# Kernel tuning notes

Hardware: AMD Instinct MI355X
Metric: run time of the kernel (lower is better)

The kernel has to match this reference:

```python
import jax, jax.numpy as jnp
import numpy as np

B, H, A, D = 4096, 50, 32, 64          # batch, history len, neighbor count, embed_dim
NU, NV = 100000, 100000                # num users, num items
L = H + A                              # total gathered entries per node


def setup_inputs() -> dict:
    key = jax.random.key(0)
    ks = jax.random.split(key, 16)
    # embedding tables (u2e/v2e uniform(-1,1) as in module init, r2e ~ N(0,1) default)
    u2e = jax.random.uniform(ks[0], (NU, D), minval=-1.0, maxval=1.0, dtype=jnp.float32)
    v2e = jax.random.uniform(ks[1], (NV, D), minval=-1.0, maxval=1.0, dtype=jnp.float32)
    r2e = jax.random.normal(ks[2], (7, D), dtype=jnp.float32)
    relation_att = jax.random.normal(ks[3], (2 * D,), dtype=jnp.float32)
    s = 1.0 / np.sqrt(2 * D)  # torch Linear default init bound
    agg_W = jax.random.uniform(ks[4], (D, 2 * D), minval=-s, maxval=s, dtype=jnp.float32)
    agg_b = jax.random.uniform(ks[5], (D,), minval=-s, maxval=s, dtype=jnp.float32)
    lin1_W = jax.random.uniform(ks[6], (D, 2 * D), minval=-s, maxval=s, dtype=jnp.float32)
    lin1_b = jax.random.uniform(ks[7], (D,), minval=-s, maxval=s, dtype=jnp.float32)
    nodes_u = jax.random.randint(ks[8], (B,), 0, NU)
    nodes_v = jax.random.randint(ks[9], (B,), 0, NV)
    hist_u = jax.random.randint(ks[10], (B, H), 0, NV)   # user history = items
    hist_ur = jax.random.randint(ks[11], (B, H), 0, 6)   # ratings 0..5
    adj_u = jax.random.randint(ks[12], (B, A), 0, NU)    # social neighbors = users
    hist_v = jax.random.randint(ks[13], (B, H), 0, NU)   # item history = users
    hist_vr = jax.random.randint(ks[14], (B, H), 0, 6)
    adj_v = jax.random.randint(ks[15], (B, A), 0, NV)    # item-adj neighbors = items
    return dict(u2e=u2e, v2e=v2e, r2e=r2e, relation_att=relation_att,
                agg_W=agg_W, agg_b=agg_b, lin1_W=lin1_W, lin1_b=lin1_b,
                nodes_u=nodes_u, nodes_v=nodes_v,
                hist_u=hist_u, hist_ur=hist_ur, adj_u=adj_u,
                hist_v=hist_v, hist_vr=hist_vr, adj_v=adj_v)


def _encode(node_tab, target_tab, hist_tab, neigh_tab, r2e, relation_att,
            agg_W, agg_b, lin1_W, lin1_b, nodes, targets, hn, hr, adj):
    # Node_Encoder.forward + Node_Aggregator (percent=1.0 -> deterministic:
    # multinomial selects all indices; softmax-weighted sum is permutation-invariant).
    nf = node_tab[nodes]                                   # [B, D]
    tf = target_tab[targets]                               # [B, D]
    # query (computed as in original; with percent=1 the norm-softmax sampling
    # probability does not affect the output)
    _q = jnp.concatenate([nf, tf], axis=-1) @ agg_W.T + agg_b  # [B, D]
    hist_feat = jnp.concatenate([hist_tab[hn], neigh_tab[adj]], axis=1)  # [B, L, D]
    rates = jnp.concatenate([hr, jnp.full(adj.shape, 6, dtype=hr.dtype)], axis=1)
    rate_feat = r2e[rates]                                 # [B, L, D]
    sel = jnp.concatenate([hist_feat, rate_feat], axis=-1)  # [B, L, 2D]
    logits = jnp.einsum('ble,e->bl', sel, relation_att)    # [B, L]
    p = jax.nn.softmax(logits, axis=1)                     # softmax2 over entries
    neigh = jnp.einsum('bl,bld->bd', p, hist_feat)         # weighted sum [B, D]
    comb = jnp.concatenate([nf, neigh], axis=-1)           # [B, 2D]
    return jax.nn.relu(comb @ lin1_W.T + lin1_b)           # [B, D]


def reference(u2e, v2e, r2e, relation_att, agg_W, agg_b, lin1_W, lin1_b,
              nodes_u, nodes_v, hist_u, hist_ur, adj_u, hist_v, hist_vr, adj_v):
    # user side: isitem=False -> node=u2e, target=v2e, hist=v2e, neighbor=u2e
    eu = _encode(u2e, v2e, v2e, u2e, r2e, relation_att, agg_W, agg_b, lin1_W, lin1_b,
                 nodes_u, nodes_v, hist_u, hist_ur, adj_u)
    # item side: isitem=True -> node=v2e, target=u2e, hist=u2e, neighbor=v2e
    ev = _encode(v2e, u2e, u2e, v2e, r2e, relation_att, agg_W, agg_b, lin1_W, lin1_b,
                 nodes_v, nodes_u, hist_v, hist_vr, adj_v)
    return jnp.sum(eu * ev, axis=1)                        # [B]
```

## Files before the change

### kernel.cpp

```cpp
#include <hip/hip_runtime.h>


typedef _Float16 half4v __attribute__((ext_vector_type(4)));

#define NB 4096
#define NH 50
#define NA 32
#define ND 64
#define NROWS 100000


__global__ __launch_bounds__(256) void convert_f16(const float* __restrict__ src,
                                                   _Float16* __restrict__ dst,
                                                   int n4)
{
    int i = blockIdx.x * blockDim.x + threadIdx.x;
    const int stride = gridDim.x * blockDim.x;
    const float4* s4 = (const float4*)src;
    half4v* d4 = (half4v*)dst;
    for (; i < n4; i += stride) {
        const float4 v = s4[i];
        half4v h;
        h.x = (_Float16)v.x; h.y = (_Float16)v.y;
        h.z = (_Float16)v.z; h.w = (_Float16)v.w;
        d4[i] = h;
    }
}

__global__ void rlog_setup(const float* __restrict__ r2e,
                           const float* __restrict__ ra,
                           float* __restrict__ ws_rlog)
{
    const int lane = threadIdx.x;
    const float ra_hi = ra[64 + lane];
    #pragma unroll
    for (int r = 0; r < 7; ++r) {
        float part = r2e[r * 64 + lane] * ra_hi;
        #pragma unroll
        for (int off = 32; off >= 1; off >>= 1)
            part += __shfl_xor(part, off);
        if (lane == 0) ws_rlog[r] = part;
    }
}


__global__ __launch_bounds__(256, 8) void graphconsis_f16(
    const float* __restrict__ u2e, const float* __restrict__ v2e,
    const _Float16* __restrict__ uh, const _Float16* __restrict__ vh,
    const float* __restrict__ ra,
    const float* __restrict__ lin1_W, const float* __restrict__ lin1_b,
    const int* __restrict__ nodes_u, const int* __restrict__ nodes_v,
    const int* __restrict__ hist_u, const int* __restrict__ hist_ur,
    const int* __restrict__ adj_u,
    const int* __restrict__ hist_v, const int* __restrict__ hist_vr,
    const int* __restrict__ adj_v,
    const float* __restrict__ ws_rlog,
    float* __restrict__ out)
{
    __shared__ float lds_comb[4][128];
    __shared__ float ed[4][64];

    const int wid  = threadIdx.x >> 6;
    const int lane = threadIdx.x & 63;
    const int g    = lane >> 4;
    const int j    = lane & 15;
    const int side = wid >> 1;
    const int b    = __builtin_amdgcn_readfirstlane(blockIdx.x * 2 + (wid & 1));

    const float* nodeTab      = side ? v2e : u2e;
    const _Float16* histTab   = side ? uh : vh;
    const _Float16* neighTab  = side ? vh : uh;
    const int* nodes = side ? nodes_v : nodes_u;
    const int* hn    = side ? hist_v  : hist_u;
    const int* hr    = side ? hist_vr : hist_ur;
    const int* adj   = side ? adj_v   : adj_u;

    const float4 ra4  = *(const float4*)(ra + 4 * j);
    const float rlog6 = ws_rlog[6];

    int hidx[13];
    #pragma unroll
    for (int k = 0; k < 13; ++k) {
        int l = 4 * k + g; if (l > NH - 1) l = NH - 1;
        hidx[k] = hn[b * NH + l];
    }
    float rl0 = 0.f;
    { int l = 4 * j + g; if (l < NH) rl0 = ws_rlog[hr[b * NH + l]]; }

    float ssum = 0.f;
    float4 acc = make_float4(0.f, 0.f, 0.f, 0.f);

    #pragma unroll 4
    for (int k = 0; k < 12; ++k) {
        const half4v eh = *(const half4v*)(histTab + hidx[k] * ND + 4 * j);
        const float4 e = make_float4((float)eh.x, (float)eh.y, (float)eh.z, (float)eh.w);
        float part = e.x * ra4.x;
        part = fmaf(e.y, ra4.y, part);
        part = fmaf(e.z, ra4.z, part);
        part = fmaf(e.w, ra4.w, part);
        part += (j == k) ? rl0 : 0.f;
        part += __shfl_xor(part, 1);
        part += __shfl_xor(part, 2);
        part += __shfl_xor(part, 4);
        part += __shfl_xor(part, 8);
        const float p = __expf(part);
        ssum += p;
        acc.x = fmaf(p, e.x, acc.x);
        acc.y = fmaf(p, e.y, acc.y);
        acc.z = fmaf(p, e.z, acc.z);
        acc.w = fmaf(p, e.w, acc.w);
    }
    {
        const half4v eh = *(const half4v*)(histTab + hidx[12] * ND + 4 * j);
        const float4 e = make_float4((float)eh.x, (float)eh.y, (float)eh.z, (float)eh.w);
        float part = e.x * ra4.x;
        part = fmaf(e.y, ra4.y, part);
        part = fmaf(e.z, ra4.z, part);
        part = fmaf(e.w, ra4.w, part);
        part += (j == 12) ? rl0 : 0.f;
        part += __shfl_xor(part, 1);
        part += __shfl_xor(part, 2);
        part += __shfl_xor(part, 4);
        part += __shfl_xor(part, 8);
        const float p = (g < 2) ? __expf(part) : 0.f;
        ssum += p;
        acc.x = fmaf(p, e.x, acc.x);
        acc.y = fmaf(p, e.y, acc.y);
        acc.z = fmaf(p, e.z, acc.z);
        acc.w = fmaf(p, e.w, acc.w);
    }
    #pragma unroll 4
    for (int k = 0; k < 8; ++k) {
        const int idx = adj[b * NA + 4 * k + g];
        const half4v eh = *(const half4v*)(neighTab + idx * ND + 4 * j);
        const float4 e = make_float4((float)eh.x, (float)eh.y, (float)eh.z, (float)eh.w);
        float part = e.x * ra4.x;
        part = fmaf(e.y, ra4.y, part);
        part = fmaf(e.z, ra4.z, part);
        part = fmaf(e.w, ra4.w, part);
        part += __shfl_xor(part, 1);
        part += __shfl_xor(part, 2);
        part += __shfl_xor(part, 4);
        part += __shfl_xor(part, 8);
        const float p = __expf(part + rlog6);
        ssum += p;
        acc.x = fmaf(p, e.x, acc.x);
        acc.y = fmaf(p, e.y, acc.y);
        acc.z = fmaf(p, e.z, acc.z);
        acc.w = fmaf(p, e.w, acc.w);
    }

    ssum += __shfl_xor(ssum, 16);
    ssum += __shfl_xor(ssum, 32);
    acc.x += __shfl_xor(acc.x, 16); acc.x += __shfl_xor(acc.x, 32);
    acc.y += __shfl_xor(acc.y, 16); acc.y += __shfl_xor(acc.y, 32);
    acc.z += __shfl_xor(acc.z, 16); acc.z += __shfl_xor(acc.z, 32);
    acc.w += __shfl_xor(acc.w, 16); acc.w += __shfl_xor(acc.w, 32);

    const float inv = 1.0f / ssum;
    const float4 nf4 = *(const float4*)(nodeTab + nodes[b] * ND + 4 * j);

    if (g == 0) {
        *(float4*)&lds_comb[wid][4 * j] = nf4;
        float4 n4 = make_float4(acc.x * inv, acc.y * inv, acc.z * inv, acc.w * inv);
        *(float4*)&lds_comb[wid][64 + 4 * j] = n4;
    }

    float o = lin1_b[lane];
    const float4* W4 = (const float4*)(lin1_W + lane * 128);
    const float4* C4 = (const float4*)lds_comb[wid];
    #pragma unroll 8
    for (int kk = 0; kk < 32; ++kk) {
        const float4 w = W4[kk];
        const float4 c = C4[kk];
        o = fmaf(w.x, c.x, o);
        o = fmaf(w.y, c.y, o);
        o = fmaf(w.z, c.z, o);
        o = fmaf(w.w, c.w, o);
    }
    const float evec = fmaxf(o, 0.f);

    ed[wid][lane] = evec;
    __syncthreads();

    if (wid < 2) {
        float prod = ed[wid][lane] * ed[wid + 2][lane];
        #pragma unroll
        for (int off = 32; off >= 1; off >>= 1)
            prod += __shfl_xor(prod, off);
        if (lane == 0) out[blockIdx.x * 2 + wid] = prod;
    }
}


__global__ __launch_bounds__(256, 8) void graphconsis_f32(
    const float* __restrict__ u2e, const float* __restrict__ v2e,
    const float* __restrict__ ra,
    const float* __restrict__ lin1_W, const float* __restrict__ lin1_b,
    const int* __restrict__ nodes_u, const int* __restrict__ nodes_v,
    const int* __restrict__ hist_u, const int* __restrict__ hist_ur,
    const int* __restrict__ adj_u,
    const int* __restrict__ hist_v, const int* __restrict__ hist_vr,
    const int* __restrict__ adj_v,
    const float* __restrict__ ws_rlog,
    float* __restrict__ out)
{
    __shared__ float lds_comb[4][128];
    __shared__ float ed[4][64];

    const int wid  = threadIdx.x >> 6;
    const int lane = threadIdx.x & 63;
    const int g    = lane >> 4;
    const int j    = lane & 15;
    const int side = wid >> 1;
    const int b    = __builtin_amdgcn_readfirstlane(blockIdx.x * 2 + (wid & 1));

    const float* nodeTab  = side ? v2e : u2e;
    const float* histTab  = side ? u2e : v2e;
    const float* neighTab = side ? v2e : u2e;
    const int* nodes = side ? nodes_v : nodes_u;
    const int* hn    = side ? hist_v  : hist_u;
    const int* hr    = side ? hist_vr : hist_ur;
    const int* adj   = side ? adj_v   : adj_u;

    const float4 ra4  = *(const float4*)(ra + 4 * j);
    const float rlog6 = ws_rlog[6];

    int hidx[13];
    #pragma unroll
    for (int k = 0; k < 13; ++k) {
        int l = 4 * k + g; if (l > NH - 1) l = NH - 1;
        hidx[k] = hn[b * NH + l];
    }
    float rl0 = 0.f;
    { int l = 4 * j + g; if (l < NH) rl0 = ws_rlog[hr[b * NH + l]]; }

    float ssum = 0.f;
    float4 acc = make_float4(0.f, 0.f, 0.f, 0.f);

    #pragma unroll 4
    for (int k = 0; k < 12; ++k) {
        const float4 e = *(const float4*)(histTab + hidx[k] * ND + 4 * j);
        float part = e.x * ra4.x;
        part = fmaf(e.y, ra4.y, part);
        part = fmaf(e.z, ra4.z, part);
        part = fmaf(e.w, ra4.w, part);
        part += (j == k) ? rl0 : 0.f;
        part += __shfl_xor(part, 1);
        part += __shfl_xor(part, 2);
        part += __shfl_xor(part, 4);
        part += __shfl_xor(part, 8);
        const float p = __expf(part);
        ssum += p;
        acc.x = fmaf(p, e.x, acc.x);
        acc.y = fmaf(p, e.y, acc.y);
        acc.z = fmaf(p, e.z, acc.z);
        acc.w = fmaf(p, e.w, acc.w);
    }
    {
        const float4 e = *(const float4*)(histTab + hidx[12] * ND + 4 * j);
        float part = e.x * ra4.x;
        part = fmaf(e.y, ra4.y, part);
        part = fmaf(e.z, ra4.z, part);
        part = fmaf(e.w, ra4.w, part);
        part += (j == 12) ? rl0 : 0.f;
        part += __shfl_xor(part, 1);
        part += __shfl_xor(part, 2);
        part += __shfl_xor(part, 4);
        part += __shfl_xor(part, 8);
        const float p = (g < 2) ? __expf(part) : 0.f;
        ssum += p;
        acc.x = fmaf(p, e.x, acc.x);
        acc.y = fmaf(p, e.y, acc.y);
        acc.z = fmaf(p, e.z, acc.z);
        acc.w = fmaf(p, e.w, acc.w);
    }
    #pragma unroll 4
    for (int k = 0; k < 8; ++k) {
        const int idx = adj[b * NA + 4 * k + g];
        const float4 e = *(const float4*)(neighTab + idx * ND + 4 * j);
        float part = e.x * ra4.x;
        part = fmaf(e.y, ra4.y, part);
        part = fmaf(e.z, ra4.z, part);
        part = fmaf(e.w, ra4.w, part);
        part += __shfl_xor(part, 1);
        part += __shfl_xor(part, 2);
        part += __shfl_xor(part, 4);
        part += __shfl_xor(part, 8);
        const float p = __expf(part + rlog6);
        ssum += p;
        acc.x = fmaf(p, e.x, acc.x);
        acc.y = fmaf(p, e.y, acc.y);
        acc.z = fmaf(p, e.z, acc.z);
        acc.w = fmaf(p, e.w, acc.w);
    }

    ssum += __shfl_xor(ssum, 16);
    ssum += __shfl_xor(ssum, 32);
    acc.x += __shfl_xor(acc.x, 16); acc.x += __shfl_xor(acc.x, 32);
    acc.y += __shfl_xor(acc.y, 16); acc.y += __shfl_xor(acc.y, 32);
    acc.z += __shfl_xor(acc.z, 16); acc.z += __shfl_xor(acc.z, 32);
    acc.w += __shfl_xor(acc.w, 16); acc.w += __shfl_xor(acc.w, 32);

    const float inv = 1.0f / ssum;
    const float4 nf4 = *(const float4*)(nodeTab + nodes[b] * ND + 4 * j);

    if (g == 0) {
        *(float4*)&lds_comb[wid][4 * j] = nf4;
        float4 n4 = make_float4(acc.x * inv, acc.y * inv, acc.z * inv, acc.w * inv);
        *(float4*)&lds_comb[wid][64 + 4 * j] = n4;
    }

    float o = lin1_b[lane];
    const float4* W4 = (const float4*)(lin1_W + lane * 128);
    const float4* C4 = (const float4*)lds_comb[wid];
    #pragma unroll 8
    for (int kk = 0; kk < 32; ++kk) {
        const float4 w = W4[kk];
        const float4 c = C4[kk];
        o = fmaf(w.x, c.x, o);
        o = fmaf(w.y, c.y, o);
        o = fmaf(w.z, c.z, o);
        o = fmaf(w.w, c.w, o);
    }
    const float evec = fmaxf(o, 0.f);

    ed[wid][lane] = evec;
    __syncthreads();

    if (wid < 2) {
        float prod = ed[wid][lane] * ed[wid + 2][lane];
        #pragma unroll
        for (int off = 32; off >= 1; off >>= 1)
            prod += __shfl_xor(prod, off);
        if (lane == 0) out[blockIdx.x * 2 + wid] = prod;
    }
}


extern "C" void kernel_launch(void* const* d_in, const int* in_sizes, int n_in,
                              void* d_out, int out_size, void* d_ws, size_t ws_size,
                              hipStream_t stream)
{
    const float* u2e     = (const float*)d_in[0];
    const float* v2e     = (const float*)d_in[1];
    const float* r2e     = (const float*)d_in[2];
    const float* ra      = (const float*)d_in[3];
    const float* lin1_W  = (const float*)d_in[6];
    const float* lin1_b  = (const float*)d_in[7];
    const int* nodes_u   = (const int*)d_in[8];
    const int* nodes_v   = (const int*)d_in[9];
    const int* hist_u    = (const int*)d_in[10];
    const int* hist_ur   = (const int*)d_in[11];
    const int* adj_u     = (const int*)d_in[12];
    const int* hist_v    = (const int*)d_in[13];
    const int* hist_vr   = (const int*)d_in[14];
    const int* adj_v     = (const int*)d_in[15];
    float* out = (float*)d_out;

    const size_t tab_elems = (size_t)NROWS * ND;
    const size_t f16_bytes = tab_elems * sizeof(_Float16);
    const size_t need = 2 * f16_bytes + 64;

    if (ws_size >= need) {
        _Float16* uh = (_Float16*)d_ws;
        _Float16* vh = (_Float16*)((char*)d_ws + f16_bytes);
        float* ws_rlog = (float*)((char*)d_ws + 2 * f16_bytes);
        const int n4 = (int)(tab_elems / 4);
        hipLaunchKernelGGL(convert_f16, dim3(2048), dim3(256), 0, stream, u2e, uh, n4);
        hipLaunchKernelGGL(convert_f16, dim3(2048), dim3(256), 0, stream, v2e, vh, n4);
        hipLaunchKernelGGL(rlog_setup, dim3(1), dim3(64), 0, stream, r2e, ra, ws_rlog);
        hipLaunchKernelGGL(graphconsis_f16, dim3(NB / 2), dim3(256), 0, stream,
                           u2e, v2e, uh, vh, ra, lin1_W, lin1_b,
                           nodes_u, nodes_v, hist_u, hist_ur, adj_u,
                           hist_v, hist_vr, adj_v, ws_rlog, out);
    } else {
        float* ws_rlog = (float*)d_ws;
        hipLaunchKernelGGL(rlog_setup, dim3(1), dim3(64), 0, stream, r2e, ra, ws_rlog);
        hipLaunchKernelGGL(graphconsis_f32, dim3(NB / 2), dim3(256), 0, stream,
                           u2e, v2e, ra, lin1_W, lin1_b,
                           nodes_u, nodes_v, hist_u, hist_ur, adj_u,
                           hist_v, hist_vr, adj_v, ws_rlog, out);
    }
}
```

Before: 64.08 us.

## Merge table conversions, inline rating logits, prefetch all gathers into registers

The two f16 conversion launches are merged into one kernel that uses nontemporal loads, and the separate rlog_setup launch is removed. Each wave now recomputes the seven rating logits itself using wave shuffles. The main kernel issues all history, neighbour and node-row gathers up front into register arrays for more memory-level parallelism. Launch bounds are relaxed to allow higher register use. This cuts kernel launches and serial dependency stalls, at the cost of redundant per-wave logit math and possibly lower occupancy.

```diff
diff --git a/kernel.cpp b/kernel.cpp
--- a/kernel.cpp
+++ b/kernel.cpp
@@ -2,6 +2,7 @@
 
 
 typedef _Float16 half4v __attribute__((ext_vector_type(4)));
+typedef float f32x4 __attribute__((ext_vector_type(4)));
 
 #define NB 4096
 #define NH 50
@@ -10,51 +11,40 @@
 #define NROWS 100000
 
 
-__global__ __launch_bounds__(256) void convert_f16(const float* __restrict__ src,
-                                                   _Float16* __restrict__ dst,
-                                                   int n4)
+__global__ __launch_bounds__(256) void convert_f16_both(
+    const float* __restrict__ u2e, const float* __restrict__ v2e,
+    _Float16* __restrict__ uh, _Float16* __restrict__ vh, int n4_per)
 {
     int i = blockIdx.x * blockDim.x + threadIdx.x;
     const int stride = gridDim.x * blockDim.x;
-    const float4* s4 = (const float4*)src;
-    half4v* d4 = (half4v*)dst;
-    for (; i < n4; i += stride) {
-        const float4 v = s4[i];
+    const f32x4* su = (const f32x4*)u2e;
+    const f32x4* sv = (const f32x4*)v2e;
+    half4v* du = (half4v*)uh;
+    half4v* dv = (half4v*)vh;
+    for (; i < 2 * n4_per; i += stride) {
+        const bool second = (i >= n4_per);
+        const f32x4* s = second ? sv : su;
+        half4v* d = second ? dv : du;
+        const int k = second ? (i - n4_per) : i;
+        const f32x4 v = __builtin_nontemporal_load(&s[k]);
         half4v h;
         h.x = (_Float16)v.x; h.y = (_Float16)v.y;
         h.z = (_Float16)v.z; h.w = (_Float16)v.w;
-        d4[i] = h;
+        d[k] = h;
     }
 }
 
-__global__ void rlog_setup(const float* __restrict__ r2e,
-                           const float* __restrict__ ra,
-                           float* __restrict__ ws_rlog)
-{
-    const int lane = threadIdx.x;
-    const float ra_hi = ra[64 + lane];
-    #pragma unroll
-    for (int r = 0; r < 7; ++r) {
-        float part = r2e[r * 64 + lane] * ra_hi;
-        #pragma unroll
-        for (int off = 32; off >= 1; off >>= 1)
-            part += __shfl_xor(part, off);
-        if (lane == 0) ws_rlog[r] = part;
-    }
-}
-
-
-__global__ __launch_bounds__(256, 8) void graphconsis_f16(
+
+__global__ __launch_bounds__(256, 2) void graphconsis_f16(
     const float* __restrict__ u2e, const float* __restrict__ v2e,
     const _Float16* __restrict__ uh, const _Float16* __restrict__ vh,
-    const float* __restrict__ ra,
+    const float* __restrict__ r2e, const float* __restrict__ ra,
     const float* __restrict__ lin1_W, const float* __restrict__ lin1_b,
     const int* __restrict__ nodes_u, const int* __restrict__ nodes_v,
     const int* __restrict__ hist_u, const int* __restrict__ hist_ur,
     const int* __restrict__ adj_u,
     const int* __restrict__ hist_v, const int* __restrict__ hist_vr,
     const int* __restrict__ adj_v,
-    const float* __restrict__ ws_rlog,
     float* __restrict__ out)
 {
     __shared__ float lds_comb[4][128];
@@ -67,16 +57,15 @@
     const int side = wid >> 1;
     const int b    = __builtin_amdgcn_readfirstlane(blockIdx.x * 2 + (wid & 1));
 
-    const float* nodeTab      = side ? v2e : u2e;
-    const _Float16* histTab   = side ? uh : vh;
-    const _Float16* neighTab  = side ? vh : uh;
+    const float* nodeTab     = side ? v2e : u2e;
+    const _Float16* histTab  = side ? uh : vh;
+    const _Float16* neighTab = side ? vh : uh;
     const int* nodes = side ? nodes_v : nodes_u;
     const int* hn    = side ? hist_v  : hist_u;
     const int* hr    = side ? hist_vr : hist_ur;
     const int* adj   = side ? adj_v   : adj_u;
 
-    const float4 ra4  = *(const float4*)(ra + 4 * j);
-    const float rlog6 = ws_rlog[6];
+    const float4 ra4 = *(const float4*)(ra + 4 * j);
 
     int hidx[13];
     #pragma unroll
@@ -84,15 +73,55 @@
         int l = 4 * k + g; if (l > NH - 1) l = NH - 1;
         hidx[k] = hn[b * NH + l];
     }
-    float rl0 = 0.f;
-    { int l = 4 * j + g; if (l < NH) rl0 = ws_rlog[hr[b * NH + l]]; }
+    int aidx[8];
+    #pragma unroll
+    for (int k = 0; k < 8; ++k)
+        aidx[k] = adj[b * NA + 4 * k + g];
+    int hrv = 6;
+    { int l = 4 * j + g; if (l < NH) hrv = hr[b * NH + l]; }
+
+    const float4 nf4 = *(const float4*)(nodeTab + nodes[b] * ND + 4 * j);
+    half4v rh[13];
+    #pragma unroll
+    for (int k = 0; k < 13; ++k)
+        rh[k] = *(const half4v*)(histTab + hidx[k] * ND + 4 * j);
+    half4v raj[8];
+    #pragma unroll
+    for (int k = 0; k < 8; ++k)
+        raj[k] = *(const half4v*)(neighTab + aidx[k] * ND + 4 * j);
+
+    const float ra_hi = ra[64 + lane];
+    float r0, r1, r2, r3, r4, r5, r6;
+    {
+        float t[7];
+        #pragma unroll
+        for (int r = 0; r < 7; ++r) {
+            float part = r2e[r * 64 + lane] * ra_hi;
+            part += __shfl_xor(part, 1);
+            part += __shfl_xor(part, 2);
+            part += __shfl_xor(part, 4);
+            part += __shfl_xor(part, 8);
+            part += __shfl_xor(part, 16);
+            part += __shfl_xor(part, 32);
+            t[r] = part;
+        }
+        r0 = t[0]; r1 = t[1]; r2 = t[2]; r3 = t[3]; r4 = t[4]; r5 = t[5]; r6 = t[6];
+    }
+    float rl0 = r6;
+    rl0 = (hrv == 0) ? r0 : rl0;
+    rl0 = (hrv == 1) ? r1 : rl0;
+    rl0 = (hrv == 2) ? r2 : rl0;
+    rl0 = (hrv == 3) ? r3 : rl0;
+    rl0 = (hrv == 4) ? r4 : rl0;
+    rl0 = (hrv == 5) ? r5 : rl0;
+    const float rlog6 = r6;
 
     float ssum = 0.f;
     float4 acc = make_float4(0.f, 0.f, 0.f, 0.f);
 
-    #pragma unroll 4
+    #pragma unroll
     for (int k = 0; k < 12; ++k) {
-        const half4v eh = *(const half4v*)(histTab + hidx[k] * ND + 4 * j);
+        const half4v eh = rh[k];
         const float4 e = make_float4((float)eh.x, (float)eh.y, (float)eh.z, (float)eh.w);
         float part = e.x * ra4.x;
         part = fmaf(e.y, ra4.y, part);
@@ -111,7 +140,7 @@
         acc.w = fmaf(p, e.w, acc.w);
     }
     {
-        const half4v eh = *(const half4v*)(histTab + hidx[12] * ND + 4 * j);
+        const half4v eh = rh[12];
         const float4 e = make_float4((float)eh.x, (float)eh.y, (float)eh.z, (float)eh.w);
         float part = e.x * ra4.x;
         part = fmaf(e.y, ra4.y, part);
@@ -129,10 +158,9 @@
         acc.z = fmaf(p, e.z, acc.z);
         acc.w = fmaf(p, e.w, acc.w);
     }
-    #pragma unroll 4
+    #pragma unroll
     for (int k = 0; k < 8; ++k) {
-        const int idx = adj[b * NA + 4 * k + g];
-        const half4v eh = *(const half4v*)(neighTab + idx * ND + 4 * j);
+        const half4v eh = raj[k];
         const float4 e = make_float4((float)eh.x, (float)eh.y, (float)eh.z, (float)eh.w);
         float part = e.x * ra4.x;
         part = fmaf(e.y, ra4.y, part);
@@ -158,7 +186,6 @@
     acc.w += __shfl_xor(acc.w, 16); acc.w += __shfl_xor(acc.w, 32);
 
     const float inv = 1.0f / ssum;
-    const float4 nf4 = *(const float4*)(nodeTab + nodes[b] * ND + 4 * j);
 
     if (g == 0) {
         *(float4*)&lds_comb[wid][4 * j] = nf4;
@@ -193,18 +220,18 @@
 }
 
 
-__global__ __launch_bounds__(256, 8) void graphconsis_f32(
+__global__ __launch_bounds__(256) void graphconsis_f32(
     const float* __restrict__ u2e, const float* __restrict__ v2e,
-    const float* __restrict__ ra,
+    const float* __restrict__ r2e, const float* __restrict__ ra,
     const float* __restrict__ lin1_W, const float* __restrict__ lin1_b,
     const int* __restrict__ nodes_u, const int* __restrict__ nodes_v,
     const int* __restrict__ hist_u, const int* __restrict__ hist_ur,
     const int* __restrict__ adj_u,
     const int* __restrict__ hist_v, const int* __restrict__ hist_vr,
     const int* __restrict__ adj_v,
-    const float* __restrict__ ws_rlog,
     float* __restrict__ out)
 {
+    __shared__ float rlog_lds[8];
     __shared__ float lds_comb[4][128];
     __shared__ float ed[4][64];
 
@@ -223,8 +250,7 @@
     const int* hr    = side ? hist_vr : hist_ur;
     const int* adj   = side ? adj_v   : adj_u;
 
-    const float4 ra4  = *(const float4*)(ra + 4 * j);
-    const float rlog6 = ws_rlog[6];
+    const float4 ra4 = *(const float4*)(ra + 4 * j);
 
     int hidx[13];
     #pragma unroll
@@ -232,15 +258,46 @@
         int l = 4 * k + g; if (l > NH - 1) l = NH - 1;
         hidx[k] = hn[b * NH + l];
     }
-    float rl0 = 0.f;
-    { int l = 4 * j + g; if (l < NH) rl0 = ws_rlog[hr[b * NH + l]]; }
+    int aidx[8];
+    #pragma unroll
+    for (int k = 0; k < 8; ++k)
+        aidx[k] = adj[b * NA + 4 * k + g];
+    int hrv = 7;
+    { int l = 4 * j + g; if (l < NH) hrv = hr[b * NH + l]; }
+
+    const float4 nf4 = *(const float4*)(nodeTab + nodes[b] * ND + 4 * j);
+    float4 rh[13];
+    #pragma unroll
+    for (int k = 0; k < 13; ++k)
+        rh[k] = *(const float4*)(histTab + hidx[k] * ND + 4 * j);
+    float4 raj[8];
+    #pragma unroll
+    for (int k = 0; k < 8; ++k)
+        raj[k] = *(const float4*)(neighTab + aidx[k] * ND + 4 * j);
+
+    if (wid == 0) {
+        const float ra_hi = ra[64 + lane];
+        #pragma unroll
+        for (int r = 0; r < 7; ++r) {
+            float part = r2e[r * 64 + lane] * ra_hi;
+            #pragma unroll
+            for (int off = 32; off >= 1; off >>= 1)
+                part += __shfl_xor(part, off);
+            if (lane == 0) rlog_lds[r] = part;
+        }
+        if (lane == 0) rlog_lds[7] = 0.f;
+    }
+    __syncthreads();
+
+    const float rl0   = rlog_lds[hrv];
+    const float rlog6 = rlog_lds[6];
 
     float ssum = 0.f;
     float4 acc = make_float4(0.f, 0.f, 0.f, 0.f);
 
-    #pragma unroll 4
+    #pragma unroll
     for (int k = 0; k < 12; ++k) {
-        const float4 e = *(const float4*)(histTab + hidx[k] * ND + 4 * j);
+        const float4 e = rh[k];
         float part = e.x * ra4.x;
         part = fmaf(e.y, ra4.y, part);
         part = fmaf(e.z, ra4.z, part);
@@ -258,7 +315,7 @@
         acc.w = fmaf(p, e.w, acc.w);
     }
     {
-        const float4 e = *(const float4*)(histTab + hidx[12] * ND + 4 * j);
+        const float4 e = rh[12];
         float part = e.x * ra4.x;
         part = fmaf(e.y, ra4.y, part);
         part = fmaf(e.z, ra4.z, part);
@@ -275,10 +332,9 @@
         acc.z = fmaf(p, e.z, acc.z);
         acc.w = fmaf(p, e.w, acc.w);
     }
-    #pragma unroll 4
+    #pragma unroll
     for (int k = 0; k < 8; ++k) {
-        const int idx = adj[b * NA + 4 * k + g];
-        const float4 e = *(const float4*)(neighTab + idx * ND + 4 * j);
+        const float4 e = raj[k];
         float part = e.x * ra4.x;
         part = fmaf(e.y, ra4.y, part);
         part = fmaf(e.z, ra4.z, part);
@@ -303,7 +359,6 @@
     acc.w += __shfl_xor(acc.w, 16); acc.w += __shfl_xor(acc.w, 32);
 
     const float inv = 1.0f / ssum;
-    const float4 nf4 = *(const float4*)(nodeTab + nodes[b] * ND + 4 * j);
 
     if (g == 0) {
         *(float4*)&lds_comb[wid][4 * j] = nf4;
@@ -360,26 +415,22 @@
 
     const size_t tab_elems = (size_t)NROWS * ND;
     const size_t f16_bytes = tab_elems * sizeof(_Float16);
-    const size_t need = 2 * f16_bytes + 64;
+    const size_t need = 2 * f16_bytes;
 
     if (ws_size >= need) {
         _Float16* uh = (_Float16*)d_ws;
         _Float16* vh = (_Float16*)((char*)d_ws + f16_bytes);
-        float* ws_rlog = (float*)((char*)d_ws + 2 * f16_bytes);
-        const int n4 = (int)(tab_elems / 4);
-        hipLaunchKernelGGL(convert_f16, dim3(2048), dim3(256), 0, stream, u2e, uh, n4);
-        hipLaunchKernelGGL(convert_f16, dim3(2048), dim3(256), 0, stream, v2e, vh, n4);
-        hipLaunchKernelGGL(rlog_setup, dim3(1), dim3(64), 0, stream, r2e, ra, ws_rlog);
+        const int n4_per = (int)(tab_elems / 4);
+        hipLaunchKernelGGL(convert_f16_both, dim3(4096), dim3(256), 0, stream,
+                           u2e, v2e, uh, vh, n4_per);
         hipLaunchKernelGGL(graphconsis_f16, dim3(NB / 2), dim3(256), 0, stream,
-                           u2e, v2e, uh, vh, ra, lin1_W, lin1_b,
+                           u2e, v2e, uh, vh, r2e, ra, lin1_W, lin1_b,
                            nodes_u, nodes_v, hist_u, hist_ur, adj_u,
-                           hist_v, hist_vr, adj_v, ws_rlog, out);
+                           hist_v, hist_vr, adj_v, out);
     } else {
-        float* ws_rlog = (float*)d_ws;
-        hipLaunchKernelGGL(rlog_setup, dim3(1), dim3(64), 0, stream, r2e, ra, ws_rlog);
         hipLaunchKernelGGL(graphconsis_f32, dim3(NB / 2), dim3(256), 0, stream,
-                           u2e, v2e, ra, lin1_W, lin1_b,
+                           u2e, v2e, r2e, ra, lin1_W, lin1_b,
                            nodes_u, nodes_v, hist_u, hist_ur, adj_u,
-                           hist_v, hist_vr, adj_v, ws_rlog, out);
+                           hist_v, hist_vr, adj_v, out);
     }
 }
```

After: 63.79 us. About the same (-0.4%).
